# Kernel optimization log

Hardware: AMD Instinct MI355X
Metric: run time of the kernel (lower is better)

Reference implementation:

```python
import jax, jax.numpy as jnp
import numpy as np

H = 64          # hidden_dim
L = 3           # num_layers
R = 5           # relations: 0=acts_on, 1=uses, 2=rev_uses, 3=at, 4=rev_at
N_CRIME = 20


def _sage(x_src, x_dst, src, dst, Wl, bl, Wr):
    """PyG SAGEConv (mean aggr): lin_l(mean_j x_src[j]) + lin_r(x_dst)."""
    n_dst = x_dst.shape[0]
    msg = x_src[src]                                               # [E, H] gather
    agg = jax.ops.segment_sum(msg, dst, num_segments=n_dst)        # [N_dst, H]
    cnt = jax.ops.segment_sum(jnp.ones(src.shape, x_src.dtype), dst, num_segments=n_dst)
    mean = agg / jnp.maximum(cnt, 1.0)[:, None]                    # isolated nodes -> 0
    return mean @ Wl.T + bl + x_dst @ Wr.T


def setup_inputs() -> dict:
    key = jax.random.key(0)
    ks = jax.random.split(key, 24)
    N_P, N_O, N_L = 200_000, 100_000, 50_000
    E = 1_000_000
    V_P, V_O, V_L = 250_000, 120_000, 60_000
    s = 0.05
    ri = lambda k, n, hi: jax.random.randint(k, (n,), 0, hi)
    rn = lambda k, shp: jax.random.normal(k, shp, dtype=jnp.float32) * s
    return {
        'x_person': ri(ks[0], N_P, V_P),
        'x_object': ri(ks[1], N_O, V_O),
        'x_location': ri(ks[2], N_L, V_L),
        'acts_src': ri(ks[3], E, N_P), 'acts_dst': ri(ks[4], E, N_P),
        'uses_src': ri(ks[5], E, N_P), 'uses_dst': ri(ks[6], E, N_O),
        'at_src':   ri(ks[7], E, N_P), 'at_dst':   ri(ks[8], E, N_L),
        'person_emb':   rn(ks[9],  (V_P, H)),
        'object_emb':   rn(ks[10], (V_O, H)),
        'location_emb': rn(ks[11], (V_L, H)),
        'Wl': rn(ks[12], (L, R, H, H)),   # lin_l weights per layer per relation
        'bl': rn(ks[13], (L, R, H)),      # lin_l biases
        'Wr': rn(ks[14], (L, R, H, H)),   # lin_r (root) weights, no bias
        'Wc1': rn(ks[15], (H, 3 * H)), 'bc1': rn(ks[16], (H,)),
        'Wc2': rn(ks[17], (N_CRIME, H)), 'bc2': rn(ks[18], (N_CRIME,)),
        'Ws1': rn(ks[19], (H // 2, H)), 'bs1': rn(ks[20], (H // 2,)),
        'Ws2': rn(ks[21], (1, H // 2)), 'bs2': rn(ks[22], (1,)),
    }


def reference(x_person, x_object, x_location,
              acts_src, acts_dst, uses_src, uses_dst, at_src, at_dst,
              person_emb, object_emb, location_emb,
              Wl, bl, Wr, Wc1, bc1, Wc2, bc2, Ws1, bs1, Ws2, bs2):
    p = person_emb[x_person]        # [N_P, H]
    o = object_emb[x_object]        # [N_O, H]
    l = location_emb[x_location]    # [N_L, H]
    for t in range(L):
        W, b, Wroot = Wl[t], bl[t], Wr[t]
        # person receives from acts_on, rev_uses (flipped uses), rev_at (flipped at);
        # HeteroConv(aggr='mean') averages the per-relation outputs.
        p_new = (_sage(p, p, acts_src, acts_dst, W[0], b[0], Wroot[0])
                 + _sage(o, p, uses_dst, uses_src, W[2], b[2], Wroot[2])
                 + _sage(l, p, at_dst, at_src, W[4], b[4], Wroot[4])) / 3.0
        o_new = _sage(p, o, uses_src, uses_dst, W[1], b[1], Wroot[1])
        l_new = _sage(p, l, at_src, at_dst, W[3], b[3], Wroot[3])
        # dropout is identity at inference; relu + residual
        p = jax.nn.relu(p_new) + p
        o = jax.nn.relu(o_new) + o
        l = jax.nn.relu(l_new) + l
    g = jnp.concatenate([p.mean(0), o.mean(0), l.mean(0)])        # [3H]
    h = jax.nn.relu(g @ Wc1.T + bc1)
    crime_logits = h @ Wc2.T + bc2                                 # [N_CRIME]
    s = jax.nn.relu(p @ Ws1.T + bs1)
    suspect_scores = (s @ Ws2.T + bs2)[:, 0]                       # [N_P]
    return jnp.concatenate([crime_logits, suspect_scores])        # [N_CRIME + N_P]
```

## Files before the change

### kernel.cpp

```cpp
#include <hip/hip_runtime.h>

typedef unsigned short u16;
typedef unsigned int u32;
typedef __attribute__((ext_vector_type(8))) short bf16x8;
typedef __attribute__((ext_vector_type(4))) float f32x4;

#define BKW 2048
#define BKSH 11
#define MAXBK 512

__device__ __forceinline__ float bf2f(u16 u) { return __uint_as_float(((u32)u) << 16); }
__device__ __forceinline__ u16 f2bf(float f) {
  u32 u = __float_as_uint(f);
  return (u16)((u + 0x7fffu + ((u >> 16) & 1u)) >> 16);
}

__global__ void gather_f2b(const float* __restrict__ emb, const int* __restrict__ ids,
                           u16* __restrict__ out, int n, int V) {
  int u = blockIdx.x * 256 + threadIdx.x;
  if (u >= n * 16) return;
  int node = u >> 4, q = u & 15;
  int r = ids[node];
  r = ((u32)r < (u32)V) ? r : 0;
  float4 v = *(const float4*)(emb + (size_t)r * 64 + q * 4);
  ushort4 o;
  o.x = f2bf(v.x); o.y = f2bf(v.y); o.z = f2bf(v.z); o.w = f2bf(v.w);
  *(ushort4*)(out + (size_t)node * 64 + q * 4) = o;
}

__global__ void prep_w(const float* __restrict__ Wl, const float* __restrict__ Wr,
                       const float* __restrict__ bl,
                       u16* __restrict__ WBlin, u16* __restrict__ WBroot,
                       float* __restrict__ bsums) {
  int i = blockIdx.x * 256 + threadIdx.x;
  const int TL = 3 * 5 * 4096;
  if (i < TL) { WBlin[i] = f2bf(Wl[i]); return; }
  int j = i - TL;
  if (j < 3 * 3 * 4096) {
    int lt = j / (3 * 4096), rem = j % (3 * 4096), c = rem / 4096, e = rem % 4096;
    int r0 = (c == 0) ? 0 : (c == 1) ? 1 : 3;
    float v = Wr[((size_t)lt * 5 + r0) * 4096 + e];
    if (c == 0) v += Wr[((size_t)lt * 5 + 2) * 4096 + e] +
                     Wr[((size_t)lt * 5 + 4) * 4096 + e];
    WBroot[j] = f2bf(v);
    return;
  }
  int k2 = j - 3 * 3 * 4096;
  if (k2 < 3 * 3 * 64) {
    int lt = k2 / 192, rem = k2 % 192, c = rem / 64, e = rem % 64;
    int r0 = (c == 0) ? 0 : (c == 1) ? 1 : 3;
    float v = bl[((size_t)lt * 5 + r0) * 64 + e];
    if (c == 0) v += bl[((size_t)lt * 5 + 2) * 64 + e] +
                     bl[((size_t)lt * 5 + 4) * 64 + e];
    bsums[k2] = v;
  }
}

__global__ void __launch_bounds__(256) bkt_count(
    const int* __restrict__ D0, const int* __restrict__ D1, const int* __restrict__ D2,
    const int* __restrict__ D3, const int* __restrict__ D4,
    int* __restrict__ bcnt,
    int E1, int E2, int E3, int E4, int E5,
    int s1, int s2, int s3, int s4,
    int N0, int N1, int N2, int N3, int N4, int NBK) {
  __shared__ int c[MAXBK];
  int t = threadIdx.x;
  for (int i = t; i < NBK; i += 256) c[i] = 0;
  __syncthreads();
  int chunk0 = blockIdx.x * 8192;
  for (int j = 0; j < 32; j++) {
    int e = chunk0 + j * 256 + t;
    if (e >= E5) break;
    const int* dp; int sb, N, le;
    if (e < E1)      { dp = D0; sb = 0;  N = N0; le = e; }
    else if (e < E2) { dp = D1; sb = s1; N = N1; le = e - E1; }
    else if (e < E3) { dp = D2; sb = s2; N = N2; le = e - E2; }
    else if (e < E4) { dp = D3; sb = s3; N = N3; le = e - E3; }
    else             { dp = D4; sb = s4; N = N4; le = e - E4; }
    int d = dp[le];
    if ((u32)d < (u32)N) atomicAdd(&c[sb + (d >> BKSH)], 1);
  }
  __syncthreads();
  for (int i = t; i < NBK; i += 256) if (c[i]) atomicAdd(&bcnt[i], c[i]);
}

__global__ void __launch_bounds__(512) bkt_scan(
    const int* __restrict__ bcnt, int* __restrict__ bbase, int* __restrict__ bcur,
    int* __restrict__ off,
    int s1, int s2, int s3, int s4, int NBK,
    int q0, int q1, int q2, int q3, int q4) {
  __shared__ int sb[MAXBK + 1];
  __shared__ int ws[8];
  int t = threadIdx.x, lane = t & 63, wv = t >> 6;
  int v = (t < NBK) ? bcnt[t] : 0;
  int s = v;
  #pragma unroll
  for (int d = 1; d < 64; d <<= 1) { int u = __shfl_up(s, d); if (lane >= d) s += u; }
  if (lane == 63) ws[wv] = s;
  __syncthreads();
  int wbase = 0;
  for (int i = 0; i < wv; i++) wbase += ws[i];
  int excl = wbase + (s - v);
  if (t < NBK) { bbase[t] = excl; bcur[t] = excl; sb[t] = excl; }
  if (t == 0) {
    int tot = 0;
    #pragma unroll
    for (int i = 0; i < 8; i++) tot += ws[i];
    bbase[NBK] = tot; sb[NBK] = tot;
  }
  __syncthreads();
  if (t == 0) off[q0] = sb[s1];
  else if (t == 1) off[q1] = sb[s2] - sb[s1];
  else if (t == 2) off[q2] = sb[s3] - sb[s2];
  else if (t == 3) off[q3] = sb[s4] - sb[s3];
  else if (t == 4) off[q4] = sb[NBK] - sb[s4];
}

__global__ void __launch_bounds__(256) bkt_scatter(
    const int* __restrict__ S0, const int* __restrict__ S1, const int* __restrict__ S2,
    const int* __restrict__ S3, const int* __restrict__ S4,
    const int* __restrict__ D0, const int* __restrict__ D1, const int* __restrict__ D2,
    const int* __restrict__ D3, const int* __restrict__ D4,
    int* __restrict__ bcur, u32* __restrict__ bdata,
    int E1, int E2, int E3, int E4, int E5,
    int s1, int s2, int s3, int s4,
    int N0, int N1, int N2, int N3, int N4, int NBK) {
  __shared__ int c[MAXBK];
  __shared__ int base[MAXBK];
  int t = threadIdx.x;
  for (int i = t; i < NBK; i += 256) c[i] = 0;
  __syncthreads();
  int chunk0 = blockIdx.x * 4096;
  int lb[16]; u32 rec[16];
  #pragma unroll
  for (int j = 0; j < 16; j++) {
    int e = chunk0 + j * 256 + t;
    lb[j] = -1;
    if (e < E5) {
      const int *sp, *dp; int sb, N, le;
      if (e < E1)      { sp = S0; dp = D0; sb = 0;  N = N0; le = e; }
      else if (e < E2) { sp = S1; dp = D1; sb = s1; N = N1; le = e - E1; }
      else if (e < E3) { sp = S2; dp = D2; sb = s2; N = N2; le = e - E2; }
      else if (e < E4) { sp = S3; dp = D3; sb = s3; N = N3; le = e - E3; }
      else             { sp = S4; dp = D4; sb = s4; N = N4; le = e - E4; }
      int d = dp[le];
      if ((u32)d < (u32)N) {
        lb[j] = sb + (d >> BKSH);
        rec[j] = ((u32)sp[le] << BKSH) | (u32)(d & (BKW - 1));
        atomicAdd(&c[lb[j]], 1);
      }
    }
  }
  __syncthreads();
  for (int i = t; i < NBK; i += 256) {
    int cc = c[i];
    base[i] = cc ? atomicAdd(&bcur[i], cc) : 0;
    c[i] = 0;
  }
  __syncthreads();
  #pragma unroll
  for (int j = 0; j < 16; j++) {
    if (lb[j] >= 0) {
      int r = atomicAdd(&c[lb[j]], 1);
      int pos = base[lb[j]] + r;
      if ((u32)pos < (u32)E5) bdata[pos] = rec[j];
    }
  }
}

__global__ void __launch_bounds__(1024) bkt_sort(
    const int* __restrict__ bbase, const u32* __restrict__ bdata,
    int* __restrict__ off, int* __restrict__ csr,
    int s1, int s2, int s3, int s4, int NBK,
    int N0, int N1, int N2, int N3, int N4,
    int o1, int o2, int o3, int o4,
    int g1, int g2, int g3, int g4,
    int La, int Lu, int Lt) {
  __shared__ int cnt[BKW];
  __shared__ int pre[BKW];
  __shared__ int wsum[16];
  int b = blockIdx.x, t = threadIdx.x, lane = t & 63, wv = t >> 6;
  int r = (b >= s4) ? 4 : (b >= s3) ? 3 : (b >= s2) ? 2 : (b >= s1) ? 1 : 0;
  int sr = (r == 0) ? 0 : (r == 1) ? s1 : (r == 2) ? s2 : (r == 3) ? s3 : s4;
  int Nr = (r == 0) ? N0 : (r == 1) ? N1 : (r == 2) ? N2 : (r == 3) ? N3 : N4;
  int oR = (r == 0) ? 0 : (r == 1) ? o1 : (r == 2) ? o2 : (r == 3) ? o3 : o4;
  int gR = (r == 0) ? 0 : (r == 1) ? g1 : (r == 2) ? g2 : (r == 3) ? g3 : g4;
  int Lr = (r == 0) ? La : (r == 1 || r == 2) ? Lu : Lt;
  int relRecBase = bbase[sr];
  int bstart = bbase[b], bend = bbase[b + 1];
  int node0 = (b - sr) << BKSH;
  int W = Nr - node0; if (W > BKW) W = BKW;
  int csrB = bstart - relRecBase;
  for (int i = t; i < BKW; i += 1024) cnt[i] = 0;
  __syncthreads();
  for (int i = bstart + t; i < bend; i += 1024)
    atomicAdd(&cnt[bdata[i] & (BKW - 1)], 1);
  __syncthreads();
  int basei = t * 2;
  int v0 = cnt[basei], v1 = cnt[basei + 1];
  int tsum = v0 + v1;
  int s = tsum;
  #pragma unroll
  for (int d = 1; d < 64; d <<= 1) { int u = __shfl_up(s, d); if (lane >= d) s += u; }
  if (lane == 63) wsum[wv] = s;
  __syncthreads();
  int wbase = 0;
  #pragma unroll
  for (int i = 0; i < 16; i++) wbase += (i < wv) ? wsum[i] : 0;
  int run = wbase + (s - tsum);
  pre[basei] = run;
  if (basei < W) off[oR + node0 + basei] = csrB + run;
  run += v0;
  pre[basei + 1] = run;
  if (basei + 1 < W) off[oR + node0 + basei + 1] = csrB + run;
  cnt[basei] = 0; cnt[basei + 1] = 0;
  __syncthreads();
  for (int i = bstart + t; i < bend; i += 1024) {
    u32 rc = bdata[i];
    int ld = rc & (BKW - 1);
    int src = (int)(rc >> BKSH);
    int rank = atomicAdd(&cnt[ld], 1);
    int pos = csrB + pre[ld] + rank;
    if ((u32)pos < (u32)Lr) csr[gR + pos] = src;
  }
}

template <int NM>
__global__ void __launch_bounds__(256, 4) sage_fused(
    const u16* __restrict__ X, u16* __restrict__ out,
    const u16* __restrict__ S0, const int* __restrict__ of0, const int* __restrict__ ix0, int ns0,
    const u16* __restrict__ S1, const int* __restrict__ of1, const int* __restrict__ ix1, int ns1,
    const u16* __restrict__ S2, const int* __restrict__ of2, const int* __restrict__ ix2, int ns2,
    const u16* __restrict__ lin0, const u16* __restrict__ lin1, const u16* __restrict__ lin2,
    const u16* __restrict__ root, const float* __restrict__ bsum,
    float scale, int n) {
  constexpr int KC = 2 * (NM + 1);
  constexpr int AP = (NM + 1) * 64 + 8;
  __shared__ __align__(16) u16 A_lds[32 * AP];
  __shared__ __align__(16) u16 D_lds[32 * 72];
  int t = threadIdx.x, wave = t >> 6, lane = t & 63;
  int m0 = blockIdx.x << 5;

  {
    int s = lane >> 3, c = lane & 7;
    int rr = wave * 8 + s;
    int g = m0 + rr;
    int gc = (g < n) ? g : (n - 1);
    #pragma unroll
    for (int rel = 0; rel < NM; rel++) {
      const u16* S  = (rel == 0) ? S0 : (rel == 1) ? S1 : S2;
      const int* of = (rel == 0) ? of0 : (rel == 1) ? of1 : of2;
      const int* ix = (rel == 0) ? ix0 : (rel == 1) ? ix1 : ix2;
      u32 ns = (u32)((rel == 0) ? ns0 : (rel == 1) ? ns1 : ns2);
      int e0 = of[gc], e1 = of[gc + 1];
      int deg = e1 - e0;
      float a[8] = {0.f, 0.f, 0.f, 0.f, 0.f, 0.f, 0.f, 0.f};
      for (int base = e0; __any(base < e1); base += 8) {
        int id[8];
        #pragma unroll
        for (int j = 0; j < 8; j++) {
          int e = base + j;
          id[j] = (e < e1) ? ix[e] : -1;
        }
        #pragma unroll
        for (int j = 0; j < 8; j++) {
          bf16x8 v = {};
          if ((u32)id[j] < ns)
            v = *(const bf16x8*)(S + (size_t)(u32)id[j] * 64 + c * 8);
          #pragma unroll
          for (int k = 0; k < 8; k++) a[k] += bf2f((u16)v[k]);
        }
      }
      float inv = (deg > 0) ? 1.f / (float)deg : 0.f;
      bf16x8 m8;
      #pragma unroll
      for (int k = 0; k < 8; k++) m8[k] = (short)f2bf(a[k] * inv);
      *(bf16x8*)&A_lds[rr * AP + rel * 64 + c * 8] = m8;
    }
    bf16x8 xv = *(const bf16x8*)(X + (size_t)gc * 64 + c * 8);
    *(bf16x8*)&A_lds[rr * AP + NM * 64 + c * 8] = xv;
  }
  __syncthreads();

  int col0 = lane & 15, kb = lane >> 4;
  int rt = (wave & 1) * 16;
  int ct = (wave >> 1) * 32;
  const u16* Wbase[KC];
  #pragma unroll
  for (int kc = 0; kc < KC; kc++) {
    int m = kc >> 1;
    const u16* basep = (m < NM) ? ((m == 0) ? lin0 : (m == 1) ? lin1 : lin2) : root;
    Wbase[kc] = basep + (kc & 1) * 32 + kb * 8;
  }
  f32x4 acc0 = {}, acc1 = {};
  #pragma unroll
  for (int kc = 0; kc < KC; kc++) {
    bf16x8 Af = *(const bf16x8*)&A_lds[(rt + col0) * AP + kc * 32 + kb * 8];
    bf16x8 B0 = *(const bf16x8*)(Wbase[kc] + (ct + col0) * 64);
    acc0 = __builtin_amdgcn_mfma_f32_16x16x32_bf16(Af, B0, acc0, 0, 0, 0);
    bf16x8 B1 = *(const bf16x8*)(Wbase[kc] + (ct + 16 + col0) * 64);
    acc1 = __builtin_amdgcn_mfma_f32_16x16x32_bf16(Af, B1, acc1, 0, 0, 0);
  }

  float b0 = bsum[ct + col0];
  float b1 = bsum[ct + 16 + col0];
  #pragma unroll
  for (int j = 0; j < 4; j++) {
    int dr = rt + kb * 4 + j;
    float xv0 = bf2f(A_lds[dr * AP + NM * 64 + ct + col0]);
    D_lds[dr * 72 + ct + col0] = f2bf(fmaxf((acc0[j] + b0) * scale, 0.f) + xv0);
    float xv1 = bf2f(A_lds[dr * AP + NM * 64 + ct + 16 + col0]);
    D_lds[dr * 72 + ct + 16 + col0] = f2bf(fmaxf((acc1[j] + b1) * scale, 0.f) + xv1);
  }
  __syncthreads();
  int row32 = t >> 3, cc = (t & 7) * 8;
  int row = m0 + row32;
  if (row < n) {
    bf16x8 o8;
    #pragma unroll
    for (int j = 0; j < 8; j++) o8[j] = (short)D_lds[row32 * 72 + cc + j];
    *(bf16x8*)(out + (size_t)row * 64 + cc) = o8;
  }
}

__global__ void __launch_bounds__(256) colsum3(const u16* __restrict__ x, int n,
                                               float* __restrict__ gout) {
  __shared__ float part[64];
  int t = threadIdx.x;
  if (t < 64) part[t] = 0.f;
  __syncthreads();
  int lane = t & 63;
  int c = (lane & 7) * 8;
  int rs = blockIdx.x * 32 + (t >> 3);
  int stride = gridDim.x * 32;
  float a[8] = {0.f, 0.f, 0.f, 0.f, 0.f, 0.f, 0.f, 0.f};
  for (int r = rs; r < n; r += stride) {
    bf16x8 v = *(const bf16x8*)(x + (size_t)r * 64 + c);
    #pragma unroll
    for (int k = 0; k < 8; k++) a[k] += bf2f((u16)v[k]);
  }
  #pragma unroll
  for (int k = 0; k < 8; k++) {
    a[k] += __shfl_xor(a[k], 8);
    a[k] += __shfl_xor(a[k], 16);
    a[k] += __shfl_xor(a[k], 32);
  }
  if (lane < 8) {
    #pragma unroll
    for (int k = 0; k < 8; k++) atomicAdd(&part[lane * 8 + k], a[k]);
  }
  __syncthreads();
  if (t < 64) atomicAdd(&gout[t], part[t]);
}

__global__ void __launch_bounds__(256) head2(const float* __restrict__ gsum,
    const float* __restrict__ Wc1, const float* __restrict__ bc1,
    const float* __restrict__ Wc2, const float* __restrict__ bc2,
    int NP, int NO, int NL, float* __restrict__ out) {
  __shared__ float g[192];
  __shared__ float h[64];
  int t = threadIdx.x;
  if (t < 192) {
    float d = (t < 64) ? (float)NP : (t < 128) ? (float)NO : (float)NL;
    g[t] = gsum[t] / d;
  }
  __syncthreads();
  if (t < 64) {
    float a = bc1[t];
    for (int k = 0; k < 192; k++) a += g[k] * Wc1[(size_t)t * 192 + k];
    h[t] = fmaxf(a, 0.f);
  }
  __syncthreads();
  if (t < 20) {
    float a = bc2[t];
    for (int k = 0; k < 64; k++) a += h[k] * Wc2[(size_t)t * 64 + k];
    out[t] = a;
  }
}

__global__ void __launch_bounds__(256) suspect2(const u16* __restrict__ p,
    const float* __restrict__ Ws1, const float* __restrict__ bs1,
    const float* __restrict__ Ws2, const float* __restrict__ bs2,
    float* __restrict__ out, int NP) {
  __shared__ float W1[2048];
  __shared__ float b1[32], w2[32];
  __shared__ float b2s;
  int t = threadIdx.x;
  #pragma unroll
  for (int i = 0; i < 8; i++) {
    int d = t + i * 256;
    W1[d] = Ws1[d];
  }
  if (t < 32) { b1[t] = bs1[t]; w2[t] = Ws2[t]; }
  if (t == 0) b2s = bs2[0];
  __syncthreads();
  int i = blockIdx.x * 256 + t;
  if (i >= NP) return;
  float x[64];
  #pragma unroll
  for (int q = 0; q < 8; q++) {
    bf16x8 v = *(const bf16x8*)(p + (size_t)i * 64 + q * 8);
    #pragma unroll
    for (int k = 0; k < 8; k++) x[q * 8 + k] = bf2f((u16)v[k]);
  }
  float sc = b2s;
  for (int j = 0; j < 32; j++) {
    float a = b1[j];
    const float* wr = &W1[j * 64];
    #pragma unroll
    for (int k = 0; k < 64; k++) a += x[k] * wr[k];
    sc += fmaxf(a, 0.f) * w2[j];
  }
  out[i] = sc;
}

extern "C" void kernel_launch(void* const* d_in, const int* in_sizes, int n_in,
                              void* d_out, int out_size, void* d_ws, size_t ws_size,
                              hipStream_t stream) {
  const int NP = in_sizes[0], NO = in_sizes[1], NL = in_sizes[2];
  const int Ea = in_sizes[3], Eu = in_sizes[5], Et = in_sizes[7];
  const int VP = in_sizes[9] / 64, VO = in_sizes[10] / 64, VL = in_sizes[11] / 64;

  const int* x_person   = (const int*)d_in[0];
  const int* x_object   = (const int*)d_in[1];
  const int* x_location = (const int*)d_in[2];
  const int* acts_src = (const int*)d_in[3];
  const int* acts_dst = (const int*)d_in[4];
  const int* uses_src = (const int*)d_in[5];
  const int* uses_dst = (const int*)d_in[6];
  const int* at_src   = (const int*)d_in[7];
  const int* at_dst   = (const int*)d_in[8];
  const float* person_emb   = (const float*)d_in[9];
  const float* object_emb   = (const float*)d_in[10];
  const float* location_emb = (const float*)d_in[11];
  const float* Wl  = (const float*)d_in[12];
  const float* bl  = (const float*)d_in[13];
  const float* Wr  = (const float*)d_in[14];
  const float* Wc1 = (const float*)d_in[15];
  const float* bc1 = (const float*)d_in[16];
  const float* Wc2 = (const float*)d_in[17];
  const float* bc2 = (const float*)d_in[18];
  const float* Ws1 = (const float*)d_in[19];
  const float* bs1 = (const float*)d_in[20];
  const float* Ws2 = (const float*)d_in[21];
  const float* bs2 = (const float*)d_in[22];
  float* out = (float*)d_out;

  int B0 = (NP + BKW - 1) >> BKSH;
  int B1 = (NO + BKW - 1) >> BKSH;
  int B3 = (NL + BKW - 1) >> BKSH;
  int s1 = B0, s2 = s1 + B1, s3 = s2 + B0, s4 = s3 + B3, NBK = s4 + B0;
  if (NBK > MAXBK) return;

  char* w = (char*)d_ws;
  auto alloc = [&](size_t bytes) { char* r = w; w += (bytes + 15) & ~(size_t)15; return r; };
  u16* pA = (u16*)alloc((size_t)NP * 128);
  u16* pB = (u16*)alloc((size_t)NP * 128);
  u16* oA = (u16*)alloc((size_t)NO * 128);
  u16* oB = (u16*)alloc((size_t)NO * 128);
  u16* lA = (u16*)alloc((size_t)NL * 128);
  u16* lB = (u16*)alloc((size_t)NL * 128);
  float* gsum = (float*)alloc(192 * 4);
  const size_t CN = (size_t)3 * NP + NO + NL;
  int* off = (int*)alloc((CN + 8) * 4);
  int* bcnt  = (int*)alloc((MAXBK) * 4);
  int* bbase = (int*)alloc((MAXBK + 1) * 4);
  int* bcur  = (int*)alloc((MAXBK) * 4);
  const int E1 = Ea, E2 = E1 + Eu, E3 = E2 + Eu, E4 = E3 + Et, E5 = E4 + Et;
  u32* bdata = (u32*)alloc((size_t)E5 * 4);
  u16* WBlin  = (u16*)alloc((size_t)3 * 5 * 4096 * 2);
  u16* WBroot = (u16*)alloc((size_t)3 * 3 * 4096 * 2);
  float* bsums = (float*)alloc((size_t)3 * 3 * 64 * 4);
  int* csr = (int*)alloc((size_t)E5 * 4);
  size_t base_need = (size_t)(w - (char*)d_ws);
  (void)n_in; (void)out_size;
  if (base_need > ws_size) return;

  int o0 = 0, o1 = NP + 1, o2 = o1 + NO + 1, o3 = o2 + NP + 1, o4 = o3 + NL + 1;
  int g1 = Ea, g2 = Ea + Eu, g3 = Ea + 2 * Eu, g4 = Ea + 2 * Eu + Et;
  int* csr0 = csr;
  int* csr1 = csr + g1;
  int* csr2 = csr + g2;
  int* csr3 = csr + g3;
  int* csr4 = csr + g4;

  hipMemsetAsync(bcnt, 0, MAXBK * sizeof(int), stream);
  hipMemsetAsync(gsum, 0, 192 * sizeof(float), stream);

  prep_w<<<387, 256, 0, stream>>>(Wl, Wr, bl, WBlin, WBroot, bsums);

  gather_f2b<<<(NP * 16 + 255) / 256, 256, 0, stream>>>(person_emb, x_person, pA, NP, VP);
  gather_f2b<<<(NO * 16 + 255) / 256, 256, 0, stream>>>(object_emb, x_object, oA, NO, VO);
  gather_f2b<<<(NL * 16 + 255) / 256, 256, 0, stream>>>(location_emb, x_location, lA, NL, VL);

  bkt_count<<<(E5 + 8191) / 8192, 256, 0, stream>>>(
      acts_dst, uses_dst, uses_src, at_dst, at_src, bcnt,
      E1, E2, E3, E4, E5, s1, s2, s3, s4, NP, NO, NP, NL, NP, NBK);
  bkt_scan<<<1, 512, 0, stream>>>(bcnt, bbase, bcur, off,
      s1, s2, s3, s4, NBK,
      o0 + NP, o1 + NO, o2 + NP, o3 + NL, o4 + NP);
  bkt_scatter<<<(E5 + 4095) / 4096, 256, 0, stream>>>(
      acts_src, uses_src, uses_dst, at_src, at_dst,
      acts_dst, uses_dst, uses_src, at_dst, at_src,
      bcur, bdata, E1, E2, E3, E4, E5, s1, s2, s3, s4, NP, NO, NP, NL, NP, NBK);
  bkt_sort<<<NBK, 1024, 0, stream>>>(bbase, bdata, off, csr,
      s1, s2, s3, s4, NBK, NP, NO, NP, NL, NP,
      o1, o2, o3, o4, g1, g2, g3, g4, Ea, Eu, Et);

  u16* pb[2] = {pA, pB};
  u16* ob[2] = {oA, oB};
  u16* lb[2] = {lA, lB};
  int cu = 0;
  for (int t = 0; t < 3; t++) {
    u16 *pi = pb[cu], *po = pb[1 - cu];
    u16 *oi = ob[cu], *oo = ob[1 - cu];
    u16 *li = lb[cu], *lo = lb[1 - cu];
    sage_fused<3><<<(NP + 31) / 32, 256, 0, stream>>>(pi, po,
        pi, off + o0, csr0, NP,
        oi, off + o2, csr2, NO,
        li, off + o4, csr4, NL,
        WBlin + ((size_t)t * 5 + 0) * 4096,
        WBlin + ((size_t)t * 5 + 2) * 4096,
        WBlin + ((size_t)t * 5 + 4) * 4096,
        WBroot + ((size_t)t * 3 + 0) * 4096,
        bsums + ((size_t)t * 3 + 0) * 64, 1.f / 3.f, NP);
    sage_fused<1><<<(NO + 31) / 32, 256, 0, stream>>>(oi, oo,
        pi, off + o1, csr1, NP,
        (const u16*)0, (const int*)0, (const int*)0, 0,
        (const u16*)0, (const int*)0, (const int*)0, 0,
        WBlin + ((size_t)t * 5 + 1) * 4096, (const u16*)0, (const u16*)0,
        WBroot + ((size_t)t * 3 + 1) * 4096,
        bsums + ((size_t)t * 3 + 1) * 64, 1.f, NO);
    sage_fused<1><<<(NL + 31) / 32, 256, 0, stream>>>(li, lo,
        pi, off + o3, csr3, NP,
        (const u16*)0, (const int*)0, (const int*)0, 0,
        (const u16*)0, (const int*)0, (const int*)0, 0,
        WBlin + ((size_t)t * 5 + 3) * 4096, (const u16*)0, (const u16*)0,
        WBroot + ((size_t)t * 3 + 2) * 4096,
        bsums + ((size_t)t * 3 + 2) * 64, 1.f, NL);
    cu = 1 - cu;
  }
  const u16* pF = pb[cu];
  const u16* oF = ob[cu];
  const u16* lF = lb[cu];

  colsum3<<<256, 256, 0, stream>>>(pF, NP, gsum);
  colsum3<<<128, 256, 0, stream>>>(oF, NO, gsum + 64);
  colsum3<<<64, 256, 0, stream>>>(lF, NL, gsum + 128);
  head2<<<1, 256, 0, stream>>>(gsum, Wc1, bc1, Wc2, bc2, NP, NO, NL, out);
  suspect2<<<(NP + 255) / 256, 256, 0, stream>>>(pF, Ws1, bs1, Ws2, bs2, out + 20, NP);
}
```

Measured before the change: 826.6 us.

## Merge per-type SAGE kernels into one launch per layer and prefetch neighbor ids

Combines the three per-node-type SAGE kernels of each layer into a single launch that dispatches on block index, and merges the three embedding gathers into one kernel. Inside the tile, the first eight neighbor indices for every relation are loaded up front together with the root features, so more independent memory loads are in flight before accumulation starts. This removes launch gaps and the tail of small grids, but the unified kernel sizes LDS for the largest case, which may lower occupancy for the single-relation tiles, and the prefetch adds register pressure.

```diff
diff --git a/kernel.cpp b/kernel.cpp
--- a/kernel.cpp
+++ b/kernel.cpp
@@ -15,11 +15,20 @@
   return (u16)((u + 0x7fffu + ((u >> 16) & 1u)) >> 16);
 }
 
-__global__ void gather_f2b(const float* __restrict__ emb, const int* __restrict__ ids,
-                           u16* __restrict__ out, int n, int V) {
+__global__ void gather3(const float* __restrict__ eP, const int* __restrict__ iP,
+                        u16* __restrict__ oP, int nP, int VP,
+                        const float* __restrict__ eO, const int* __restrict__ iO,
+                        u16* __restrict__ oO, int nO, int VO,
+                        const float* __restrict__ eL, const int* __restrict__ iL,
+                        u16* __restrict__ oL, int nL, int VL) {
   int u = blockIdx.x * 256 + threadIdx.x;
-  if (u >= n * 16) return;
-  int node = u >> 4, q = u & 15;
+  int tP = nP * 16, tO = tP + nO * 16, tL = tO + nL * 16;
+  const float* emb; const int* ids; u16* out; int V, lu;
+  if (u < tP)      { emb = eP; ids = iP; out = oP; V = VP; lu = u; }
+  else if (u < tO) { emb = eO; ids = iO; out = oO; V = VO; lu = u - tP; }
+  else if (u < tL) { emb = eL; ids = iL; out = oL; V = VL; lu = u - tO; }
+  else return;
+  int node = lu >> 4, q = lu & 15;
   int r = ids[node];
   r = ((u32)r < (u32)V) ? r : 0;
   float4 v = *(const float4*)(emb + (size_t)r * 64 + q * 4);
@@ -226,7 +235,8 @@
 }
 
 template <int NM>
-__global__ void __launch_bounds__(256, 4) sage_fused(
+__device__ __forceinline__ void sage_tile(
+    u16* A_lds, u16* D_lds, int tile,
     const u16* __restrict__ X, u16* __restrict__ out,
     const u16* __restrict__ S0, const int* __restrict__ of0, const int* __restrict__ ix0, int ns0,
     const u16* __restrict__ S1, const int* __restrict__ of1, const int* __restrict__ ix1, int ns1,
@@ -236,26 +246,50 @@
     float scale, int n) {
   constexpr int KC = 2 * (NM + 1);
   constexpr int AP = (NM + 1) * 64 + 8;
-  __shared__ __align__(16) u16 A_lds[32 * AP];
-  __shared__ __align__(16) u16 D_lds[32 * 72];
   int t = threadIdx.x, wave = t >> 6, lane = t & 63;
-  int m0 = blockIdx.x << 5;
+  int m0 = tile << 5;
 
   {
-    int s = lane >> 3, c = lane & 7;
-    int rr = wave * 8 + s;
+    int c = lane & 7;
+    int rr = wave * 8 + (lane >> 3);
     int g = m0 + rr;
     int gc = (g < n) ? g : (n - 1);
+    bf16x8 xv = *(const bf16x8*)(X + (size_t)gc * 64 + c * 8);
+    int e0s[NM], e1s[NM];
+    #pragma unroll
+    for (int rel = 0; rel < NM; rel++) {
+      const int* of = (rel == 0) ? of0 : (rel == 1) ? of1 : of2;
+      e0s[rel] = of[gc];
+      e1s[rel] = of[gc + 1];
+    }
+    int idp[NM][8];
+    #pragma unroll
+    for (int rel = 0; rel < NM; rel++) {
+      const int* ix = (rel == 0) ? ix0 : (rel == 1) ? ix1 : ix2;
+      int e0 = e0s[rel], e1 = e1s[rel];
+      #pragma unroll
+      for (int j = 0; j < 8; j++) {
+        int e = e0 + j;
+        idp[rel][j] = (e < e1) ? ix[e] : -1;
+      }
+    }
     #pragma unroll
     for (int rel = 0; rel < NM; rel++) {
       const u16* S  = (rel == 0) ? S0 : (rel == 1) ? S1 : S2;
-      const int* of = (rel == 0) ? of0 : (rel == 1) ? of1 : of2;
       const int* ix = (rel == 0) ? ix0 : (rel == 1) ? ix1 : ix2;
       u32 ns = (u32)((rel == 0) ? ns0 : (rel == 1) ? ns1 : ns2);
-      int e0 = of[gc], e1 = of[gc + 1];
+      int e0 = e0s[rel], e1 = e1s[rel];
       int deg = e1 - e0;
       float a[8] = {0.f, 0.f, 0.f, 0.f, 0.f, 0.f, 0.f, 0.f};
-      for (int base = e0; __any(base < e1); base += 8) {
+      #pragma unroll
+      for (int j = 0; j < 8; j++) {
+        bf16x8 v = {};
+        if ((u32)idp[rel][j] < ns)
+          v = *(const bf16x8*)(S + (size_t)(u32)idp[rel][j] * 64 + c * 8);
+        #pragma unroll
+        for (int k = 0; k < 8; k++) a[k] += bf2f((u16)v[k]);
+      }
+      for (int base = e0 + 8; __any(base < e1); base += 8) {
         int id[8];
         #pragma unroll
         for (int j = 0; j < 8; j++) {
@@ -277,7 +311,6 @@
       for (int k = 0; k < 8; k++) m8[k] = (short)f2bf(a[k] * inv);
       *(bf16x8*)&A_lds[rr * AP + rel * 64 + c * 8] = m8;
     }
-    bf16x8 xv = *(const bf16x8*)(X + (size_t)gc * 64 + c * 8);
     *(bf16x8*)&A_lds[rr * AP + NM * 64 + c * 8] = xv;
   }
   __syncthreads();
@@ -320,6 +353,43 @@
     #pragma unroll
     for (int j = 0; j < 8; j++) o8[j] = (short)D_lds[row32 * 72 + cc + j];
     *(bf16x8*)(out + (size_t)row * 64 + cc) = o8;
+  }
+}
+
+__global__ void __launch_bounds__(256, 4) sage_layer(
+    int bP, int bO,
+    const u16* Xp, u16* outp,
+    const u16* pS0, const int* pof0, const int* pix0, int pns0,
+    const u16* pS1, const int* pof1, const int* pix1, int pns1,
+    const u16* pS2, const int* pof2, const int* pix2, int pns2,
+    const u16* plin0, const u16* plin1, const u16* plin2,
+    const u16* proot, const float* pbsum, int nP,
+    const u16* Xo, u16* outo,
+    const u16* oS0, const int* oof0, const int* oix0, int ons0,
+    const u16* olin0, const u16* oroot, const float* obsum, int nO,
+    const u16* Xl, u16* outl,
+    const u16* lS0, const int* lof0, const int* lix0, int lns0,
+    const u16* llin0, const u16* lroot, const float* lbsum, int nL) {
+  __shared__ __align__(16) u16 A_lds[32 * 264];
+  __shared__ __align__(16) u16 D_lds[32 * 72];
+  int b = blockIdx.x;
+  if (b < bP) {
+    sage_tile<3>(A_lds, D_lds, b, Xp, outp,
+                 pS0, pof0, pix0, pns0, pS1, pof1, pix1, pns1,
+                 pS2, pof2, pix2, pns2, plin0, plin1, plin2,
+                 proot, pbsum, 1.f / 3.f, nP);
+  } else if (b < bP + bO) {
+    sage_tile<1>(A_lds, D_lds, b - bP, Xo, outo,
+                 oS0, oof0, oix0, ons0,
+                 (const u16*)0, (const int*)0, (const int*)0, 0,
+                 (const u16*)0, (const int*)0, (const int*)0, 0,
+                 olin0, (const u16*)0, (const u16*)0, oroot, obsum, 1.f, nO);
+  } else {
+    sage_tile<1>(A_lds, D_lds, b - bP - bO, Xl, outl,
+                 lS0, lof0, lix0, lns0,
+                 (const u16*)0, (const int*)0, (const int*)0, 0,
+                 (const u16*)0, (const int*)0, (const int*)0, 0,
+                 llin0, (const u16*)0, (const u16*)0, lroot, lbsum, 1.f, nL);
   }
 }
 
@@ -489,9 +559,11 @@
 
   prep_w<<<387, 256, 0, stream>>>(Wl, Wr, bl, WBlin, WBroot, bsums);
 
-  gather_f2b<<<(NP * 16 + 255) / 256, 256, 0, stream>>>(person_emb, x_person, pA, NP, VP);
-  gather_f2b<<<(NO * 16 + 255) / 256, 256, 0, stream>>>(object_emb, x_object, oA, NO, VO);
-  gather_f2b<<<(NL * 16 + 255) / 256, 256, 0, stream>>>(location_emb, x_location, lA, NL, VL);
+  int tg = (NP + NO + NL) * 16;
+  gather3<<<(tg + 255) / 256, 256, 0, stream>>>(
+      person_emb, x_person, pA, NP, VP,
+      object_emb, x_object, oA, NO, VO,
+      location_emb, x_location, lA, NL, VL);
 
   bkt_count<<<(E5 + 8191) / 8192, 256, 0, stream>>>(
       acts_dst, uses_dst, uses_src, at_dst, at_src, bcnt,
@@ -510,12 +582,15 @@
   u16* pb[2] = {pA, pB};
   u16* ob[2] = {oA, oB};
   u16* lb[2] = {lA, lB};
+  int bP = (NP + 31) / 32, bO = (NO + 31) / 32, bL = (NL + 31) / 32;
   int cu = 0;
   for (int t = 0; t < 3; t++) {
     u16 *pi = pb[cu], *po = pb[1 - cu];
     u16 *oi = ob[cu], *oo = ob[1 - cu];
     u16 *li = lb[cu], *lo = lb[1 - cu];
-    sage_fused<3><<<(NP + 31) / 32, 256, 0, stream>>>(pi, po,
+    sage_layer<<<bP + bO + bL, 256, 0, stream>>>(
+        bP, bO,
+        pi, po,
         pi, off + o0, csr0, NP,
         oi, off + o2, csr2, NO,
         li, off + o4, csr4, NL,
@@ -523,21 +598,17 @@
         WBlin + ((size_t)t * 5 + 2) * 4096,
         WBlin + ((size_t)t * 5 + 4) * 4096,
         WBroot + ((size_t)t * 3 + 0) * 4096,
-        bsums + ((size_t)t * 3 + 0) * 64, 1.f / 3.f, NP);
-    sage_fused<1><<<(NO + 31) / 32, 256, 0, stream>>>(oi, oo,
+        bsums + ((size_t)t * 3 + 0) * 64, NP,
+        oi, oo,
         pi, off + o1, csr1, NP,
-        (const u16*)0, (const int*)0, (const int*)0, 0,
-        (const u16*)0, (const int*)0, (const int*)0, 0,
-        WBlin + ((size_t)t * 5 + 1) * 4096, (const u16*)0, (const u16*)0,
+        WBlin + ((size_t)t * 5 + 1) * 4096,
         WBroot + ((size_t)t * 3 + 1) * 4096,
-        bsums + ((size_t)t * 3 + 1) * 64, 1.f, NO);
-    sage_fused<1><<<(NL + 31) / 32, 256, 0, stream>>>(li, lo,
+        bsums + ((size_t)t * 3 + 1) * 64, NO,
+        li, lo,
         pi, off + o3, csr3, NP,
-        (const u16*)0, (const int*)0, (const int*)0, 0,
-        (const u16*)0, (const int*)0, (const int*)0, 0,
-        WBlin + ((size_t)t * 5 + 3) * 4096, (const u16*)0, (const u16*)0,
+        WBlin + ((size_t)t * 5 + 3) * 4096,
         WBroot + ((size_t)t * 3 + 2) * 4096,
-        bsums + ((size_t)t * 3 + 2) * 64, 1.f, NL);
+        bsums + ((size_t)t * 3 + 2) * 64, NL);
     cu = 1 - cu;
   }
   const u16* pF = pb[cu];
```

Result: no change. 840.6 us (+1.7%).
